# Kernel tuning notes

Hardware: AMD Instinct MI355X
Metric: run time of the kernel (lower is better)

The kernel has to match this reference:

```python
import jax, jax.numpy as jnp
from jax import lax
import numpy as np

B, C, H, W = 32, 256, 56, 56
K = 3
EPS = 1e-5


def setup_inputs() -> dict:
    key = jax.random.key(0)
    k1, k2, k3, k4 = jax.random.split(key, 4)
    x = jax.random.normal(k1, (B, C, H, W), dtype=jnp.float32)
    # xavier_normal init for conv weight [C_out, C_in, K, K]
    fan_in = C * K * K
    fan_out = C * K * K
    std = float(np.sqrt(2.0 / (fan_in + fan_out)))
    w = jax.random.normal(k2, (C, C, K, K), dtype=jnp.float32) * std
    gamma = jnp.ones((C,), dtype=jnp.float32)
    beta = jnp.zeros((C,), dtype=jnp.float32)
    return {"x": x, "w": w, "gamma": gamma, "beta": beta}


def reference(x, w, gamma, beta):
    # --- Binarize (bi_act_method=0, bi_w_scale=1) ---
    bx = jnp.sign(x)                                   # activation sign
    wc = jnp.clip(w, -1.0, 1.0)                        # fp_weight.data.clamp_(-1,1)
    mean_val = jnp.mean(jnp.abs(wc))
    bw = jnp.sign(wc) * mean_val                       # sign(w) * mean(|w|)
    # --- float conv2d, stride 1, padding 1 ---
    out = lax.conv_general_dilated(
        bx, bw, window_strides=(1, 1), padding=[(1, 1), (1, 1)],
        dimension_numbers=("NCHW", "OIHW", "NCHW"))
    # --- identity shortcut (stride=1, C_in==C_out) ---
    out = out + x
    # --- BatchNorm2d (training-mode batch stats, affine) ---
    mean = jnp.mean(out, axis=(0, 2, 3), keepdims=True)
    var = jnp.var(out, axis=(0, 2, 3), keepdims=True)
    out = (out - mean) * lax.rsqrt(var + EPS)
    out = out * gamma[None, :, None, None] + beta[None, :, None, None]
    # --- ReLU ---
    return jax.nn.relu(out)
```

## Files before the change

### kernel.cpp

```cpp
#include <hip/hip_runtime.h>
#include <cstdint>

#define Bn   32
#define Cn   256
#define Hn   56
#define Wn   56
#define HWn  (Hn*Wn)
#define NPIX (Bn*HWn)
#define WELEMS (Cn*Cn*9)
#define EPSv 1e-5f

#define PR   58
#define PPLANE (PR*PR)

#define F_WPART 8
#define F_SUM   128
#define F_SQ    384
#define WPK_OFF  4096
#define WPK_SLOTS 40
#define ACT_OFF  (WPK_OFF + WPK_SLOTS*16384)
#define ACT_BYTES (Bn*PPLANE*Cn)

typedef int v4i __attribute__((ext_vector_type(4)));

#define GLOBAL_AS __attribute__((address_space(1)))
#define LDS_AS    __attribute__((address_space(3)))

__global__ void pack_all(const float* __restrict__ x,
                         const float* __restrict__ w,
                         float* __restrict__ wsf,
                         uint8_t* __restrict__ wpk,
                         uint8_t* __restrict__ act) {
    if (blockIdx.x < 784) {
        int v = blockIdx.x * 128 + threadIdx.x;
        int b = v / HWn;
        int p = v - b * HWn;
        int y = p / Wn;
        int xx = p - y * Wn;
        const float* xp = x + (size_t)b * Cn * HWn + p;
        int key = (xx + 1) & 15;
        uint32_t* dst = (uint32_t*)(act + ((size_t)(b * PR + (y + 1)) * PR + (xx + 1)) * 256);
        #pragma unroll
        for (int slot = 0; slot < 16; slot++) {
            uint32_t rr[4];
            #pragma unroll
            for (int cw = 0; cw < 4; cw++) {
                uint32_t r = 0;
                #pragma unroll
                for (int j = 0; j < 4; j++) {
                    uint32_t sgn = __float_as_uint(xp[(size_t)(slot * 16 + cw * 4 + j) * HWn]) >> 31;
                    r |= (sgn ? 0xFFu : 0x01u) << (j * 8);
                }
                rr[cw] = r;
            }
            *(uint4*)(dst + (size_t)((slot ^ key) * 4)) = make_uint4(rr[0], rr[1], rr[2], rr[3]);
        }
    } else if (blockIdx.x < 856) {
        int u = (blockIdx.x - 784) * 128 + threadIdx.x;
        int co = u / 36;
        int kc = u - co * 36;
        int t  = kc >> 2;
        int s  = kc & 3;
        const float* wp = w + (size_t)co * 2304 + t;
        uint32_t* dst = (uint32_t*)(wpk + ((size_t)kc * 256 + co) * 64);
        float sabs = 0.0f;
        #pragma unroll
        for (int cw = 0; cw < 16; cw++) {
            uint32_t r = 0;
            #pragma unroll
            for (int j = 0; j < 4; j++) {
                int ci = s * 64 + cw * 4 + j;
                float wv = wp[(size_t)ci * 9];
                sabs += fminf(fabsf(wv), 1.0f);
                r |= ((__float_as_uint(wv) >> 31) ? 0xFFu : 0x01u) << (j * 8);
            }
            dst[cw] = r;
        }
        #pragma unroll
        for (int off = 32; off; off >>= 1) sabs += __shfl_down(sabs, off);
        __shared__ float sh[2];
        if ((threadIdx.x & 63) == 0) sh[threadIdx.x >> 6] = sabs;
        __syncthreads();
        if (threadIdx.x == 0)
            wsf[F_WPART + (blockIdx.x - 784)] = sh[0] + sh[1];
    } else if (blockIdx.x < 913) {
        int hv = (blockIdx.x - 856) * 128 + threadIdx.x;
        int b = hv / 228;
        int r = hv - b * 228;
        int y, xx;
        if (r < 58)       { y = 0;  xx = r; }
        else if (r < 116) { y = 57; xx = r - 58; }
        else { int r2 = r - 116; y = 1 + (r2 >> 1); xx = (r2 & 1) * 57; }
        uint4* d = (uint4*)(act + ((size_t)(b * PR + y) * PR + xx) * 256);
        uint4 z = make_uint4(0, 0, 0, 0);
        #pragma unroll
        for (int i = 0; i < 16; i++) d[i] = z;
    } else {
        int idx = (blockIdx.x - 913) * 128 + threadIdx.x;
        wsf[F_SUM + idx] = 0.0f;
    }
}

__global__ __launch_bounds__(256, 2) void conv_mfma(
    const uint8_t* __restrict__ act, const uint8_t* __restrict__ wpk,
    const float* __restrict__ x, float* __restrict__ wsf,
    float* __restrict__ out) {
    __shared__ uint4 ldsv[3712];
    uint8_t* lds = (uint8_t*)ldsv;

    const int tid  = threadIdx.x;
    const int lane = tid & 63;
    const int wid  = tid >> 6;
    const int l15  = lane & 15;
    const int l4   = lane >> 4;

    const int bxr = blockIdx.x;
    const int bx  = (bxr & 7) * 112 + (bxr >> 3);
    const int b   = bx / 28;
    const int y0  = (bx - b * 28) * 2;

    {
        const uint8_t* src = act + ((size_t)b * PR + y0) * PR * 256;
        #pragma unroll
        for (int j = 0; j < 15; j++) {
            int c = wid + j * 4;
            if (c < 58) {
                __builtin_amdgcn_global_load_lds(
                    (const GLOBAL_AS uint32_t*)(const void*)(src + c * 1024 + lane * 16),
                    (LDS_AS uint32_t*)(void*)(lds + c * 1024),
                    16, 0, 0);
            }
        }
    }

    const uint8_t* abase = wpk + (wid * 64 + l15) * 64 + l4 * 16;

    v4i af0[4], af1[4], af2[4], af3[4];
    #pragma unroll
    for (int mi = 0; mi < 4; mi++) {
        af0[mi] = *(const v4i*)(abase + (size_t)0 * 16384 + mi * 1024);
        af1[mi] = *(const v4i*)(abase + (size_t)1 * 16384 + mi * 1024);
        af2[mi] = *(const v4i*)(abase + (size_t)2 * 16384 + mi * 1024);
        af3[mi] = *(const v4i*)(abase + (size_t)3 * 16384 + mi * 1024);
    }

    int pixb[7], key[7];
    #pragma unroll
    for (int ni = 0; ni < 7; ni++) {
        int n  = ni * 16 + l15;
        int r_ = n / 56;
        int c_ = n - r_ * 56;
        pixb[ni] = (r_ * 58 + c_) * 256;
        key[ni]  = c_ & 15;
    }

    __syncthreads();

    v4i acc[4][7] = {};

#define STEP(S, AF)                                                            \
    {                                                                          \
        v4i bf[7];                                                             \
        _Pragma("unroll")                                                      \
        for (int ni = 0; ni < 7; ni++)                                         \
            bf[ni] = *(const v4i*)(lds + pixb[ni] +                            \
                                   ((((S) * 4 + l4) ^ key[ni]) << 4));         \
        __builtin_amdgcn_s_setprio(1);                                         \
        _Pragma("unroll")                                                      \
        for (int ni = 0; ni < 7; ni++) {                                       \
            _Pragma("unroll")                                                  \
            for (int mi = 0; mi < 4; mi++)                                     \
                acc[mi][ni] = __builtin_amdgcn_mfma_i32_16x16x64_i8(           \
                    AF[mi], bf[ni], acc[mi][ni], 0, 0, 0);                     \
        }                                                                      \
        __builtin_amdgcn_s_setprio(0);                                         \
        {                                                                      \
            const uint8_t* ap = abase + (size_t)(t4 + (S) + 4) * 16384;        \
            _Pragma("unroll")                                                  \
            for (int mi = 0; mi < 4; mi++)                                     \
                AF[mi] = *(const v4i*)(ap + mi * 1024);                        \
        }                                                                      \
    }

    #pragma unroll 1
    for (int t = 0; t < 9; t++) {
        const int t4 = t * 4;
        STEP(0, af0)
        STEP(1, af1)
        STEP(2, af2)
        STEP(3, af3)
        const int wrap  = (t == 2 || t == 5);
        const int dtoff = (t == 8) ? 0 : (wrap ? 56 * 256 : 256);
        const int ddw   = (t == 8) ? 0 : (wrap ? -2 : 1);
        #pragma unroll
        for (int ni = 0; ni < 7; ni++) {
            pixb[ni] += dtoff;
            key[ni]   = (key[ni] + ddw) & 15;
        }
    }
#undef STEP

    float wabs = 0.0f;
    #pragma unroll
    for (int j = 0; j < 72; j++) wabs += wsf[F_WPART + j];
    const float mv = wabs * (1.0f / (float)WELEMS);

    const int co_w = wid * 64;
    const int pbase = b * (Cn * HWn) + y0 * 56;

    float ssum[4][4] = {}, ssq[4][4] = {};
    #pragma unroll
    for (int mi = 0; mi < 4; mi++) {
        #pragma unroll
        for (int ni = 0; ni < 7; ni++) {
            v4i a = acc[mi][ni];
            #pragma unroll
            for (int q = 0; q < 4; q++) {
                int co = co_w + mi * 16 + l4 * 4 + q;
                size_t idx = (size_t)pbase + (size_t)co * HWn + (ni * 16 + l15);
                float val = fmaf(mv, (float)a[q], x[idx]);
                out[idx] = val;
                ssum[mi][q] += val;
                ssq[mi][q]  += val * val;
            }
        }
    }
    #pragma unroll
    for (int mi = 0; mi < 4; mi++) {
        #pragma unroll
        for (int q = 0; q < 4; q++) {
            float s = ssum[mi][q], sq = ssq[mi][q];
            #pragma unroll
            for (int off = 1; off < 16; off <<= 1) {
                s  += __shfl_xor(s, off);
                sq += __shfl_xor(sq, off);
            }
            if (l15 == 0) {
                int co = co_w + mi * 16 + l4 * 4 + q;
                atomicAdd(&wsf[F_SUM + co], s);
                atomicAdd(&wsf[F_SQ  + co], sq);
            }
        }
    }
}

__global__ void epilogue_kernel(float* __restrict__ out,
                                const float* __restrict__ wsf,
                                const float* __restrict__ g,
                                const float* __restrict__ bt) {
    int plane = blockIdx.x;
    int c = plane & 255;
    const float n = (float)(Bn * HWn);
    float mean = wsf[F_SUM + c] / n;
    float var  = wsf[F_SQ + c] / n - mean * mean;
    float sc = g[c] * rsqrtf(var + EPSv);
    float sh = bt[c] - mean * sc;
    float4* o4 = (float4*)(out + (size_t)plane * HWn);
    for (int i = threadIdx.x; i < HWn / 4; i += 256) {
        float4 v = o4[i];
        v.x = fmaxf(fmaf(v.x, sc, sh), 0.0f);
        v.y = fmaxf(fmaf(v.y, sc, sh), 0.0f);
        v.z = fmaxf(fmaf(v.z, sc, sh), 0.0f);
        v.w = fmaxf(fmaf(v.w, sc, sh), 0.0f);
        o4[i] = v;
    }
}

extern "C" void kernel_launch(void* const* d_in, const int* in_sizes, int n_in,
                              void* d_out, int out_size, void* d_ws, size_t ws_size,
                              hipStream_t stream) {
    const float* x     = (const float*)d_in[0];
    const float* w     = (const float*)d_in[1];
    const float* gamma = (const float*)d_in[2];
    const float* beta  = (const float*)d_in[3];
    float* out = (float*)d_out;

    float*   wsf = (float*)d_ws;
    uint8_t* wpk = (uint8_t*)d_ws + WPK_OFF;
    uint8_t* act = (uint8_t*)d_ws + ACT_OFF;

    pack_all<<<dim3(917), dim3(128), 0, stream>>>(x, w, wsf, wpk, act);
    conv_mfma<<<dim3(896), dim3(256), 0, stream>>>(act, wpk, x, wsf, out);
    epilogue_kernel<<<dim3(Bn * Cn), dim3(256), 0, stream>>>(out, wsf, gamma, beta);
}
```

Before: 348.6 us.

## Shrink conv tile to one output row per block for higher occupancy

Each conv block now computes one output row (64 padded pixels, of which 56 are valid) instead of two rows. It stages a 3-row halo (about 44.5KB LDS instead of 58KB) and uses a 4x4 accumulator tile instead of 4x7. The weight-fragment prefetch ring drops from four buffers to two, and launch bounds are raised to 3 blocks per CU with twice as many blocks. The aim is better latency hiding through more occupancy. In exchange, halo reloads rise (3 rows staged per 1 output row instead of 4 per 2), 8 of 64 MFMA columns do wasted work, and the shorter prefetch distance can expose weight-load latency.

```diff
diff --git a/kernel.cpp b/kernel.cpp
--- a/kernel.cpp
+++ b/kernel.cpp
@@ -20,6 +20,8 @@
 #define WPK_SLOTS 40
 #define ACT_OFF  (WPK_OFF + WPK_SLOTS*16384)
 #define ACT_BYTES (Bn*PPLANE*Cn)
+
+#define STAGE_BYTES 44544
 
 typedef int v4i __attribute__((ext_vector_type(4)));
 
@@ -101,11 +103,11 @@
     }
 }
 
-__global__ __launch_bounds__(256, 2) void conv_mfma(
+__global__ __launch_bounds__(256, 3) void conv_mfma(
     const uint8_t* __restrict__ act, const uint8_t* __restrict__ wpk,
     const float* __restrict__ x, float* __restrict__ wsf,
     float* __restrict__ out) {
-    __shared__ uint4 ldsv[3712];
+    __shared__ uint4 ldsv[2816];
     uint8_t* lds = (uint8_t*)ldsv;
 
     const int tid  = threadIdx.x;
@@ -115,59 +117,56 @@
     const int l4   = lane >> 4;
 
     const int bxr = blockIdx.x;
-    const int bx  = (bxr & 7) * 112 + (bxr >> 3);
-    const int b   = bx / 28;
-    const int y0  = (bx - b * 28) * 2;
+    const int bx  = (bxr & 7) * 224 + (bxr >> 3);
+    const int b   = bx / 56;
+    const int y0  = bx - b * 56;
 
     {
-        const uint8_t* src = act + ((size_t)b * PR + y0) * PR * 256;
-        #pragma unroll
-        for (int j = 0; j < 15; j++) {
+        const uint8_t* src = act + ((size_t)(b * PR + y0) * PR) * 256;
+        #pragma unroll
+        for (int j = 0; j < 11; j++) {
             int c = wid + j * 4;
-            if (c < 58) {
-                __builtin_amdgcn_global_load_lds(
-                    (const GLOBAL_AS uint32_t*)(const void*)(src + c * 1024 + lane * 16),
-                    (LDS_AS uint32_t*)(void*)(lds + c * 1024),
-                    16, 0, 0);
-            }
+            int so = c * 1024 + lane * 16;
+            if (so > STAGE_BYTES - 16) so = STAGE_BYTES - 16;
+            __builtin_amdgcn_global_load_lds(
+                (const GLOBAL_AS uint32_t*)(const void*)(src + so),
+                (LDS_AS uint32_t*)(void*)(lds + c * 1024),
+                16, 0, 0);
         }
     }
 
     const uint8_t* abase = wpk + (wid * 64 + l15) * 64 + l4 * 16;
 
-    v4i af0[4], af1[4], af2[4], af3[4];
+    v4i af0[4], af1[4];
     #pragma unroll
     for (int mi = 0; mi < 4; mi++) {
         af0[mi] = *(const v4i*)(abase + (size_t)0 * 16384 + mi * 1024);
         af1[mi] = *(const v4i*)(abase + (size_t)1 * 16384 + mi * 1024);
-        af2[mi] = *(const v4i*)(abase + (size_t)2 * 16384 + mi * 1024);
-        af3[mi] = *(const v4i*)(abase + (size_t)3 * 16384 + mi * 1024);
-    }
-
-    int pixb[7], key[7];
-    #pragma unroll
-    for (int ni = 0; ni < 7; ni++) {
+    }
+
+    int pixb[4], key[4];
+    #pragma unroll
+    for (int ni = 0; ni < 4; ni++) {
         int n  = ni * 16 + l15;
-        int r_ = n / 56;
-        int c_ = n - r_ * 56;
-        pixb[ni] = (r_ * 58 + c_) * 256;
-        key[ni]  = c_ & 15;
+        int xx = n < 56 ? n : 55;
+        pixb[ni] = xx * 256;
+        key[ni]  = xx & 15;
     }
 
     __syncthreads();
 
-    v4i acc[4][7] = {};
-
-#define STEP(S, AF)                                                            \
+    v4i acc[4][4] = {};
+
+#define STEP(S, AF, KN)                                                        \
     {                                                                          \
-        v4i bf[7];                                                             \
+        v4i bf[4];                                                             \
         _Pragma("unroll")                                                      \
-        for (int ni = 0; ni < 7; ni++)                                         \
+        for (int ni = 0; ni < 4; ni++)                                         \
             bf[ni] = *(const v4i*)(lds + pixb[ni] +                            \
                                    ((((S) * 4 + l4) ^ key[ni]) << 4));         \
         __builtin_amdgcn_s_setprio(1);                                         \
         _Pragma("unroll")                                                      \
-        for (int ni = 0; ni < 7; ni++) {                                       \
+        for (int ni = 0; ni < 4; ni++) {                                       \
             _Pragma("unroll")                                                  \
             for (int mi = 0; mi < 4; mi++)                                     \
                 acc[mi][ni] = __builtin_amdgcn_mfma_i32_16x16x64_i8(           \
@@ -175,7 +174,7 @@
         }                                                                      \
         __builtin_amdgcn_s_setprio(0);                                         \
         {                                                                      \
-            const uint8_t* ap = abase + (size_t)(t4 + (S) + 4) * 16384;        \
+            const uint8_t* ap = abase + (size_t)(KN) * 16384;                  \
             _Pragma("unroll")                                                  \
             for (int mi = 0; mi < 4; mi++)                                     \
                 AF[mi] = *(const v4i*)(ap + mi * 1024);                        \
@@ -185,15 +184,15 @@
     #pragma unroll 1
     for (int t = 0; t < 9; t++) {
         const int t4 = t * 4;
-        STEP(0, af0)
-        STEP(1, af1)
-        STEP(2, af2)
-        STEP(3, af3)
+        STEP(0, af0, t4 + 2)
+        STEP(1, af1, t4 + 3)
+        STEP(2, af0, t4 + 4)
+        STEP(3, af1, t4 + 5)
         const int wrap  = (t == 2 || t == 5);
         const int dtoff = (t == 8) ? 0 : (wrap ? 56 * 256 : 256);
         const int ddw   = (t == 8) ? 0 : (wrap ? -2 : 1);
         #pragma unroll
-        for (int ni = 0; ni < 7; ni++) {
+        for (int ni = 0; ni < 4; ni++) {
             pixb[ni] += dtoff;
             key[ni]   = (key[ni] + ddw) & 15;
         }
@@ -212,16 +211,20 @@
     #pragma unroll
     for (int mi = 0; mi < 4; mi++) {
         #pragma unroll
-        for (int ni = 0; ni < 7; ni++) {
+        for (int ni = 0; ni < 4; ni++) {
             v4i a = acc[mi][ni];
+            int n = ni * 16 + l15;
+            bool ok = (n < 56);
             #pragma unroll
             for (int q = 0; q < 4; q++) {
                 int co = co_w + mi * 16 + l4 * 4 + q;
-                size_t idx = (size_t)pbase + (size_t)co * HWn + (ni * 16 + l15);
-                float val = fmaf(mv, (float)a[q], x[idx]);
-                out[idx] = val;
-                ssum[mi][q] += val;
-                ssq[mi][q]  += val * val;
+                size_t idx = (size_t)pbase + (size_t)co * HWn + n;
+                if (ok) {
+                    float val = fmaf(mv, (float)a[q], x[idx]);
+                    out[idx] = val;
+                    ssum[mi][q] += val;
+                    ssq[mi][q]  += val * val;
+                }
             }
         }
     }
@@ -280,6 +283,6 @@
     uint8_t* act = (uint8_t*)d_ws + ACT_OFF;
 
     pack_all<<<dim3(917), dim3(128), 0, stream>>>(x, w, wsf, wpk, act);
-    conv_mfma<<<dim3(896), dim3(256), 0, stream>>>(act, wpk, x, wsf, out);
+    conv_mfma<<<dim3(1792), dim3(256), 0, stream>>>(act, wpk, x, wsf, out);
     epilogue_kernel<<<dim3(Bn * Cn), dim3(256), 0, stream>>>(out, wsf, gamma, beta);
 }
```

Result: slower. 443.4 us (+27.2%).
